# Kernel tuning notes

Hardware: AMD Instinct MI355X
Metric: run time of the kernel (lower is better)

Reference implementation:

```python
import jax, jax.numpy as jnp
import numpy as np

STATE_DIM = 16
CHANNELS = 256
LENGTH = 8192
SAMPLE_RATE = 100.0


def setup_inputs() -> dict:
    key = jax.random.key(0)
    ks = jax.random.split(key, 4)
    fan = 1.0 / np.sqrt(CHANNELS)  # lecun-normal-ish scale, flax Dense default
    x = jax.random.normal(ks[0], (LENGTH, CHANNELS), dtype=jnp.float32)
    logA = jnp.log(1.0 + jnp.arange(STATE_DIM, dtype=jnp.float32))  # module's Ainit
    W_dt = jax.random.normal(ks[1], (CHANNELS, CHANNELS), dtype=jnp.float32) * fan
    b_dt = jnp.zeros((CHANNELS,), dtype=jnp.float32)
    W_B = jax.random.normal(ks[2], (CHANNELS, STATE_DIM), dtype=jnp.float32) * fan
    b_B = jnp.zeros((STATE_DIM,), dtype=jnp.float32)
    W_C = jax.random.normal(ks[3], (CHANNELS, STATE_DIM), dtype=jnp.float32) * fan
    b_C = jnp.zeros((STATE_DIM,), dtype=jnp.float32)
    return {"x": x, "logA": logA, "W_dt": W_dt, "b_dt": b_dt,
            "W_B": W_B, "b_B": b_B, "W_C": W_C, "b_C": b_C}


def reference(x, logA, W_dt, b_dt, W_B, b_B, W_C, b_C):
    # x: (L, C)
    A = -jnp.exp(logA)                                   # (S,)
    dt = jax.nn.softplus(1.0 / SAMPLE_RATE + x @ W_dt + b_dt)  # (L, C)
    B = 1.0 + x @ W_B + b_B                              # (L, S)
    C = x @ W_C + b_C                                    # (L, S)
    # discretize: Adiscr = exp(A * dt), shape (L, C, S)
    Adiscr = jnp.exp(dt[:, :, None] * A[None, None, :])
    # Bdiscr = exp((Adiscr - 1) * (B / A))  (faithful to source, incl. outer exp)
    Bdiscr = jnp.exp((Adiscr - 1.0) * (B / A)[:, None, :])  # (L, C, S)
    u = Bdiscr * x[:, :, None]                           # (L, C, S)

    def ssm_scan(p1, p2):
        (A1, c1), (A2, c2) = p1, p2
        return (A2 * A1, c2 + A2 * c1)

    _, h = jax.lax.associative_scan(ssm_scan, (Adiscr, u))  # h: (L, C, S)
    y = jnp.einsum('ls,lcs->lc', C, h)                    # (L, C)
    return y
```

## Files before the change

kernel.cpp:

```cpp
#include <hip/hip_runtime.h>
#include <hip/hip_bf16.h>
#include <math.h>

#define LL 8192
#define CC 256
#define SS 16
#define NJ (CC*SS)
#define GG 1024
#define TT 8
#define SEGS 16
#define PER (GG/SEGS)

#define LOG2E 1.4426950408889634f
#define LN2   0.6931471805599453f

typedef __attribute__((ext_vector_type(8))) short short8;
typedef __attribute__((ext_vector_type(4))) float floatx4;

__device__ __forceinline__ float fexp2(float v){ return __builtin_amdgcn_exp2f(v); }
__device__ __forceinline__ float flog2v(float v){ return __builtin_amdgcn_logf(v); }

__device__ __forceinline__ float softplus(float z){
    float t = fexp2(-fabsf(z) * LOG2E);
    return fmaxf(z, 0.f) + LN2 * flog2v(1.f + t);
}

__device__ __forceinline__ void load16(float* d, const float* __restrict__ p){
    *(float4*)&d[0]  = *(const float4*)&p[0];
    *(float4*)&d[4]  = *(const float4*)&p[4];
    *(float4*)&d[8]  = *(const float4*)&p[8];
    *(float4*)&d[12] = *(const float4*)&p[12];
}

__device__ __forceinline__ unsigned short f2b(float f){
    __hip_bfloat16 h = __float2bfloat16(f);
    return *(unsigned short*)&h;
}
__device__ __forceinline__ float b2f(unsigned short u){
    __hip_bfloat16 h = *(__hip_bfloat16*)&u;
    return __bfloat162float(h);
}

__global__ __launch_bounds__(256) void k_cast(
    const float* __restrict__ Wdt, const float* __restrict__ WB,
    const float* __restrict__ WC,
    unsigned short* __restrict__ wbh, unsigned short* __restrict__ wbl)
{
    const int idx = blockIdx.x*256 + threadIdx.x;
    const int k = idx & 255;
    const int n = idx >> 8;
    float v;
    if (n < 256)      v = Wdt[(size_t)k*CC + n];
    else if (n < 272) v = WB[(size_t)k*SS + (n-256)];
    else              v = WC[(size_t)k*SS + (n-272)];
    unsigned short hi = f2b(v);
    wbh[(size_t)n*256 + k] = hi;
    wbl[(size_t)n*256 + k] = f2b(v - b2f(hi));
}

#define MBM 64
#define MBN 32
#define MBK 64
#define ASTR 72

__global__ __launch_bounds__(256,4) void k_mm(
    const float* __restrict__ x,
    const unsigned short* __restrict__ wbh, const unsigned short* __restrict__ wbl,
    const float* __restrict__ bdt, const float* __restrict__ bB,
    const float* __restrict__ bC, const float* __restrict__ logA,
    float* __restrict__ dt, float* __restrict__ boa, float* __restrict__ cm)
{
    __shared__ unsigned short Ah[MBM*ASTR];
    __shared__ unsigned short Al[MBM*ASTR];
    __shared__ unsigned short Bh[MBN*ASTR];
    __shared__ unsigned short Bl[MBN*ASTR];

    const int tid  = threadIdx.x;
    const int n0   = blockIdx.x * MBN;
    const int row0 = blockIdx.y * MBM;

    const int lane = tid & 63;
    const int wv   = tid >> 6;
    const int wm   = wv >> 1;
    const int wn   = wv & 1;
    const int m16  = lane & 15;
    const int q    = lane >> 4;

    floatx4 acc[2];
    acc[0] = (floatx4){0.f,0.f,0.f,0.f};
    acc[1] = (floatx4){0.f,0.f,0.f,0.f};

    for (int k0 = 0; k0 < CC; k0 += MBK) {
        __syncthreads();
        #pragma unroll
        for (int h2 = 0; h2 < 2; h2++){
            int chunk = tid + h2*256;
            int r    = chunk >> 3;
            int koff = (chunk & 7) * 8;
            float4 f0 = *(const float4*)&x[(size_t)(row0+r)*CC + k0 + koff];
            float4 f1 = *(const float4*)&x[(size_t)(row0+r)*CC + k0 + koff + 4];
            const float* f = &f0.x;
            float fv[8] = {f0.x,f0.y,f0.z,f0.w,f1.x,f1.y,f1.z,f1.w};
            (void)f;
            unsigned short hs[8], ls[8];
            #pragma unroll
            for (int i=0;i<8;i++){
                hs[i] = f2b(fv[i]);
                ls[i] = f2b(fv[i] - b2f(hs[i]));
            }
            uint4 ph, pl;
            ph.x = (unsigned)hs[0] | ((unsigned)hs[1] << 16);
            ph.y = (unsigned)hs[2] | ((unsigned)hs[3] << 16);
            ph.z = (unsigned)hs[4] | ((unsigned)hs[5] << 16);
            ph.w = (unsigned)hs[6] | ((unsigned)hs[7] << 16);
            pl.x = (unsigned)ls[0] | ((unsigned)ls[1] << 16);
            pl.y = (unsigned)ls[2] | ((unsigned)ls[3] << 16);
            pl.z = (unsigned)ls[4] | ((unsigned)ls[5] << 16);
            pl.w = (unsigned)ls[6] | ((unsigned)ls[7] << 16);
            *(uint4*)&Ah[r*ASTR + koff] = ph;
            *(uint4*)&Al[r*ASTR + koff] = pl;
        }
        {
            int n    = tid >> 3;
            int koff = (tid & 7) * 8;
            *(uint4*)&Bh[n*ASTR + koff] = *(const uint4*)&wbh[(size_t)(n0+n)*256 + k0 + koff];
            *(uint4*)&Bl[n*ASTR + koff] = *(const uint4*)&wbl[(size_t)(n0+n)*256 + k0 + koff];
        }
        __syncthreads();

        #pragma unroll
        for (int ks = 0; ks < MBK; ks += 32) {
            short8 bh = *(const short8*)&Bh[(wn*16 + m16)*ASTR + ks + q*8];
            short8 bl = *(const short8*)&Bl[(wn*16 + m16)*ASTR + ks + q*8];
            #pragma unroll
            for (int mt = 0; mt < 2; mt++){
                short8 ah = *(const short8*)&Ah[(wm*32 + mt*16 + m16)*ASTR + ks + q*8];
                short8 al = *(const short8*)&Al[(wm*32 + mt*16 + m16)*ASTR + ks + q*8];
                acc[mt] = __builtin_amdgcn_mfma_f32_16x16x32_bf16(al, bh, acc[mt], 0, 0, 0);
                acc[mt] = __builtin_amdgcn_mfma_f32_16x16x32_bf16(ah, bl, acc[mt], 0, 0, 0);
                acc[mt] = __builtin_amdgcn_mfma_f32_16x16x32_bf16(ah, bh, acc[mt], 0, 0, 0);
            }
        }
    }

    const int col = n0 + wn*16 + m16;
    if (col < 256) {
        float bias = bdt[col];
        #pragma unroll
        for (int mt = 0; mt < 2; mt++){
            #pragma unroll
            for (int r = 0; r < 4; r++){
                int row = row0 + wm*32 + mt*16 + q*4 + r;
                dt[(size_t)row*CC + col] = softplus(0.01f + acc[mt][r] + bias);
            }
        }
    } else if (col < 272) {
        int s = col - 256;
        float A = -fexp2(logA[s] * LOG2E);
        float sc = LOG2E / A;
        float bias = bB[s];
        #pragma unroll
        for (int mt = 0; mt < 2; mt++){
            #pragma unroll
            for (int r = 0; r < 4; r++){
                int row = row0 + wm*32 + mt*16 + q*4 + r;
                boa[(size_t)row*SS + s] = (1.f + acc[mt][r] + bias) * sc;
            }
        }
    } else {
        int s = col - 272;
        float bias = bC[s];
        #pragma unroll
        for (int mt = 0; mt < 2; mt++){
            #pragma unroll
            for (int r = 0; r < 4; r++){
                int row = row0 + wm*32 + mt*16 + q*4 + r;
                cm[(size_t)row*SS + s] = acc[mt][r] + bias;
            }
        }
    }
}

__global__ __launch_bounds__(256) void k_scan1(const float* __restrict__ dt,
    const float* __restrict__ x, const float* __restrict__ boa,
    const float* __restrict__ logA,
    float* __restrict__ Ap, float* __restrict__ Hl)
{
    const int c = threadIdx.x;
    const int g = blockIdx.x;
    const int row0 = g * TT;

    __shared__ float boS[TT*SS];
    if (c < TT*SS) boS[c] = boa[(size_t)row0*SS + c];

    float Al2[SS];
    #pragma unroll
    for (int s=0;s<SS;s++) Al2[s] = -fexp2(logA[s]*LOG2E) * LOG2E;

    const float* __restrict__ dp = dt + (size_t)row0*CC + c;
    const float* __restrict__ xp = x  + (size_t)row0*CC + c;

    float Apr[SS], h[SS];
    #pragma unroll
    for (int s=0;s<SS;s++){ Apr[s]=1.f; h[s]=0.f; }

    __syncthreads();

    #pragma unroll
    for (int t=0;t<TT;t++){
        float d  = dp[t*CC];
        float xv = xp[t*CC];
        float bo[SS]; load16(bo, &boS[t*SS]);
        #pragma unroll
        for (int s=0;s<SS;s++){
            float a = fexp2(d * Al2[s]);
            float u = fexp2(fmaf(a, bo[s], -bo[s])) * xv;
            h[s] = fmaf(a, h[s], u);
            Apr[s] *= a;
        }
    }

    const size_t base = (size_t)g*NJ + c*SS;
    *(float4*)&Ap[base+0]  = make_float4(Apr[0],Apr[1],Apr[2],Apr[3]);
    *(float4*)&Ap[base+4]  = make_float4(Apr[4],Apr[5],Apr[6],Apr[7]);
    *(float4*)&Ap[base+8]  = make_float4(Apr[8],Apr[9],Apr[10],Apr[11]);
    *(float4*)&Ap[base+12] = make_float4(Apr[12],Apr[13],Apr[14],Apr[15]);
    *(float4*)&Hl[base+0]  = make_float4(h[0],h[1],h[2],h[3]);
    *(float4*)&Hl[base+4]  = make_float4(h[4],h[5],h[6],h[7]);
    *(float4*)&Hl[base+8]  = make_float4(h[8],h[9],h[10],h[11]);
    *(float4*)&Hl[base+12] = make_float4(h[12],h[13],h[14],h[15]);
}

__global__ __launch_bounds__(256) void k_carry(const float* __restrict__ Ap,
    const float* __restrict__ Hl, float* __restrict__ Cr)
{
    const int tid = threadIdx.x;
    const int jl  = tid & 15;
    const int seg = tid >> 4;
    const int j   = blockIdx.x * 16 + jl;

    const size_t base = (size_t)(seg*PER)*NJ + j;

    float Aag = 1.f, Uag = 0.f;
    for (int k0 = 0; k0 < PER; k0 += 8) {
        float a[8], u[8];
        #pragma unroll
        for (int i=0;i<8;i++){
            a[i] = Ap[base + (size_t)(k0+i)*NJ];
            u[i] = Hl[base + (size_t)(k0+i)*NJ];
        }
        #pragma unroll
        for (int i=0;i<8;i++){ Uag = fmaf(a[i], Uag, u[i]); Aag *= a[i]; }
    }

    __shared__ float As[SEGS][17], Us[SEGS][17];
    As[seg][jl] = Aag; Us[seg][jl] = Uag;
    __syncthreads();
    float hin = 0.f;
    for (int t = 0; t < seg; ++t)
        hin = fmaf(As[t][jl], hin, Us[t][jl]);

    float h = hin;
    for (int k0 = 0; k0 < PER; k0 += 8) {
        float a[8], u[8];
        #pragma unroll
        for (int i=0;i<8;i++){
            a[i] = Ap[base + (size_t)(k0+i)*NJ];
            u[i] = Hl[base + (size_t)(k0+i)*NJ];
        }
        #pragma unroll
        for (int i=0;i<8;i++){
            Cr[base + (size_t)(k0+i)*NJ] = h;
            h = fmaf(a[i], h, u[i]);
        }
    }
}

__global__ __launch_bounds__(256) void k_scan2(const float* __restrict__ dt,
    const float* __restrict__ x, const float* __restrict__ boa,
    const float* __restrict__ cmat, const float* __restrict__ logA,
    const float* __restrict__ Cr, float* __restrict__ y)
{
    const int c = threadIdx.x;
    const int g = blockIdx.x;
    const int row0 = g * TT;

    __shared__ float boS[TT*SS], cmS[TT*SS];
    if (c < TT*SS)       boS[c]        = boa [(size_t)row0*SS + c];
    else                 cmS[c-TT*SS]  = cmat[(size_t)row0*SS + (c-TT*SS)];

    float Al2[SS];
    #pragma unroll
    for (int s=0;s<SS;s++) Al2[s] = -fexp2(logA[s]*LOG2E) * LOG2E;

    const float* __restrict__ dp = dt + (size_t)row0*CC + c;
    const float* __restrict__ xp = x  + (size_t)row0*CC + c;
    float* __restrict__ yp = y + (size_t)row0*CC + c;

    float h[SS];
    load16(h, &Cr[(size_t)g*NJ + c*SS]);

    __syncthreads();

    #pragma unroll
    for (int t=0;t<TT;t++){
        float d  = dp[t*CC];
        float xv = xp[t*CC];
        float bo[SS]; load16(bo, &boS[t*SS]);
        float cmv[SS]; load16(cmv, &cmS[t*SS]);
        float yv = 0.f;
        #pragma unroll
        for (int s=0;s<SS;s++){
            float a = fexp2(d * Al2[s]);
            float u = fexp2(fmaf(a, bo[s], -bo[s])) * xv;
            h[s] = fmaf(a, h[s], u);
            yv = fmaf(cmv[s], h[s], yv);
        }
        yp[t*CC] = yv;
    }
}

extern "C" void kernel_launch(void* const* d_in, const int* in_sizes, int n_in,
                              void* d_out, int out_size, void* d_ws, size_t ws_size,
                              hipStream_t stream) {
    const float* x    = (const float*)d_in[0];
    const float* logA = (const float*)d_in[1];
    const float* W_dt = (const float*)d_in[2];
    const float* b_dt = (const float*)d_in[3];
    const float* W_B  = (const float*)d_in[4];
    const float* b_B  = (const float*)d_in[5];
    const float* W_C  = (const float*)d_in[6];
    const float* b_C  = (const float*)d_in[7];
    float* y  = (float*)d_out;
    float* ws = (float*)d_ws;

    float* dt  = ws;
    float* boa = dt  + (size_t)LL*CC;
    float* cmv = boa + (size_t)LL*SS;
    float* Ap  = cmv + (size_t)LL*SS;
    float* Hl  = Ap  + (size_t)GG*NJ;
    float* Cr  = Hl  + (size_t)GG*NJ;
    unsigned short* wbh = (unsigned short*)(Cr + (size_t)GG*NJ);
    unsigned short* wbl = wbh + 288*256;

    hipLaunchKernelGGL(k_cast, dim3(288), dim3(256), 0, stream, W_dt, W_B, W_C, wbh, wbl);
    hipLaunchKernelGGL(k_mm,   dim3(9,128), dim3(256), 0, stream,
                       x, wbh, wbl, b_dt, b_B, b_C, logA, dt, boa, cmv);
    hipLaunchKernelGGL(k_scan1, dim3(GG),    dim3(256), 0, stream,
                       dt, x, boa, logA, Ap, Hl);
    hipLaunchKernelGGL(k_carry, dim3(NJ/16), dim3(256), 0, stream, Ap, Hl, Cr);
    hipLaunchKernelGGL(k_scan2, dim3(GG),    dim3(256), 0, stream,
                       dt, x, boa, cmv, logA, Cr, y);
}
```

Before: 138.6 us.

## Merge chunk scan and carry pass into single-pass decoupled look-back scan

Replaces the k_scan1 and k_carry kernels with one kernel, k_scanA. Each block scans 128 rows for 16 channels using data staged in shared memory, publishes its block aggregate, and then looks back at predecessor blocks through flags to get its incoming carry. It writes per-8-row carries directly. This removes the global round trip of the Ap and Hl intermediates and one kernel launch. In exchange it adds spin-wait synchronisation and a flag memset, and it relies on predecessor blocks being scheduled so that forward progress holds.

```diff
diff --git a/kernel.cpp b/kernel.cpp
--- a/kernel.cpp
+++ b/kernel.cpp
@@ -6,10 +6,11 @@
 #define CC 256
 #define SS 16
 #define NJ (CC*SS)
-#define GG 1024
+#define GG2 1024
 #define TT 8
-#define SEGS 16
-#define PER (GG/SEGS)
+#define GCH 64
+#define CROWS 128
+#define NCB 16
 
 #define LOG2E 1.4426950408889634f
 #define LN2   0.6931471805599453f
@@ -99,9 +100,7 @@
             int koff = (chunk & 7) * 8;
             float4 f0 = *(const float4*)&x[(size_t)(row0+r)*CC + k0 + koff];
             float4 f1 = *(const float4*)&x[(size_t)(row0+r)*CC + k0 + koff + 4];
-            const float* f = &f0.x;
             float fv[8] = {f0.x,f0.y,f0.z,f0.w,f1.x,f1.y,f1.z,f1.w};
-            (void)f;
             unsigned short hs[8], ls[8];
             #pragma unroll
             for (int i=0;i<8;i++){
@@ -181,98 +180,116 @@
     }
 }
 
-__global__ __launch_bounds__(256) void k_scan1(const float* __restrict__ dt,
-    const float* __restrict__ x, const float* __restrict__ boa,
-    const float* __restrict__ logA,
-    float* __restrict__ Ap, float* __restrict__ Hl)
-{
-    const int c = threadIdx.x;
-    const int g = blockIdx.x;
-    const int row0 = g * TT;
-
-    __shared__ float boS[TT*SS];
-    if (c < TT*SS) boS[c] = boa[(size_t)row0*SS + c];
-
-    float Al2[SS];
-    #pragma unroll
-    for (int s=0;s<SS;s++) Al2[s] = -fexp2(logA[s]*LOG2E) * LOG2E;
-
-    const float* __restrict__ dp = dt + (size_t)row0*CC + c;
-    const float* __restrict__ xp = x  + (size_t)row0*CC + c;
-
-    float Apr[SS], h[SS];
-    #pragma unroll
-    for (int s=0;s<SS;s++){ Apr[s]=1.f; h[s]=0.f; }
-
-    __syncthreads();
-
-    #pragma unroll
-    for (int t=0;t<TT;t++){
-        float d  = dp[t*CC];
-        float xv = xp[t*CC];
-        float bo[SS]; load16(bo, &boS[t*SS]);
-        #pragma unroll
-        for (int s=0;s<SS;s++){
-            float a = fexp2(d * Al2[s]);
-            float u = fexp2(fmaf(a, bo[s], -bo[s])) * xv;
-            h[s] = fmaf(a, h[s], u);
-            Apr[s] *= a;
-        }
-    }
-
-    const size_t base = (size_t)g*NJ + c*SS;
-    *(float4*)&Ap[base+0]  = make_float4(Apr[0],Apr[1],Apr[2],Apr[3]);
-    *(float4*)&Ap[base+4]  = make_float4(Apr[4],Apr[5],Apr[6],Apr[7]);
-    *(float4*)&Ap[base+8]  = make_float4(Apr[8],Apr[9],Apr[10],Apr[11]);
-    *(float4*)&Ap[base+12] = make_float4(Apr[12],Apr[13],Apr[14],Apr[15]);
-    *(float4*)&Hl[base+0]  = make_float4(h[0],h[1],h[2],h[3]);
-    *(float4*)&Hl[base+4]  = make_float4(h[4],h[5],h[6],h[7]);
-    *(float4*)&Hl[base+8]  = make_float4(h[8],h[9],h[10],h[11]);
-    *(float4*)&Hl[base+12] = make_float4(h[12],h[13],h[14],h[15]);
-}
-
-__global__ __launch_bounds__(256) void k_carry(const float* __restrict__ Ap,
-    const float* __restrict__ Hl, float* __restrict__ Cr)
+__global__ __launch_bounds__(256) void k_scanA(
+    const float* __restrict__ dt, const float* __restrict__ x,
+    const float* __restrict__ boa, const float* __restrict__ logA,
+    float2* __restrict__ agg, float* __restrict__ pref,
+    int* __restrict__ flags, float* __restrict__ Cr)
 {
     const int tid = threadIdx.x;
-    const int jl  = tid & 15;
-    const int seg = tid >> 4;
-    const int j   = blockIdx.x * 16 + jl;
-
-    const size_t base = (size_t)(seg*PER)*NJ + j;
-
-    float Aag = 1.f, Uag = 0.f;
-    for (int k0 = 0; k0 < PER; k0 += 8) {
-        float a[8], u[8];
-        #pragma unroll
-        for (int i=0;i<8;i++){
-            a[i] = Ap[base + (size_t)(k0+i)*NJ];
-            u[i] = Hl[base + (size_t)(k0+i)*NJ];
-        }
-        #pragma unroll
-        for (int i=0;i<8;i++){ Uag = fmaf(a[i], Uag, u[i]); Aag *= a[i]; }
-    }
-
-    __shared__ float As[SEGS][17], Us[SEGS][17];
-    As[seg][jl] = Aag; Us[seg][jl] = Uag;
+    const int cb  = blockIdx.x;
+    const int g   = blockIdx.y;
+    const int row0 = g * CROWS;
+
+    __shared__ float dtS[CROWS*16], xS[CROWS*16], boS[CROWS*16];
+    __shared__ int sf[4];
+
+    for (int i = tid; i < CROWS*16; i += 256) {
+        int l = i >> 4, ch = i & 15;
+        dtS[i] = dt [(size_t)(row0+l)*CC + cb*16 + ch];
+        xS[i]  = x  [(size_t)(row0+l)*CC + cb*16 + ch];
+        boS[i] = boa[(size_t)(row0+l)*SS + ch];
+    }
+
+    const int cl = tid >> 4;
+    const int s  = tid & 15;
+    const float als = -fexp2(logA[s]*LOG2E) * LOG2E;
+
     __syncthreads();
-    float hin = 0.f;
-    for (int t = 0; t < seg; ++t)
-        hin = fmaf(As[t][jl], hin, Us[t][jl]);
-
-    float h = hin;
-    for (int k0 = 0; k0 < PER; k0 += 8) {
-        float a[8], u[8];
-        #pragma unroll
-        for (int i=0;i<8;i++){
-            a[i] = Ap[base + (size_t)(k0+i)*NJ];
-            u[i] = Hl[base + (size_t)(k0+i)*NJ];
-        }
-        #pragma unroll
-        for (int i=0;i<8;i++){
-            Cr[base + (size_t)(k0+i)*NJ] = h;
-            h = fmaf(a[i], h, u[i]);
-        }
+
+    float subA[16], subU[16];
+    #pragma unroll
+    for (int i=0;i<16;i++){
+        float A = 1.f, U = 0.f;
+        #pragma unroll
+        for (int r=0;r<8;r++){
+            int l = i*8 + r;
+            float d  = dtS[l*16 + cl];
+            float xv = xS [l*16 + cl];
+            float bo = boS[l*16 + s];
+            float a = fexp2(d * als);
+            float u = fexp2(fmaf(a, bo, -bo)) * xv;
+            U = fmaf(a, U, u);
+            A *= a;
+        }
+        subA[i] = A; subU[i] = U;
+    }
+    float Ablk = 1.f, Ublk = 0.f;
+    #pragma unroll
+    for (int i=0;i<16;i++){ Ublk = fmaf(subA[i], Ublk, subU[i]); Ablk *= subA[i]; }
+
+    const int fb = cb * GCH;
+    const size_t myidx = (size_t)(fb + g)*256 + tid;
+
+    if (g > 0) {
+        agg[myidx] = make_float2(Ablk, Ublk);
+        __threadfence();
+        __syncthreads();
+        if (tid == 0)
+            __hip_atomic_store(&flags[fb + g], 1, __ATOMIC_RELEASE, __HIP_MEMORY_SCOPE_AGENT);
+    }
+
+    float c0 = 0.f;
+    if (g > 0) {
+        float accA = 1.f, accU = 0.f;
+        int p = g - 1;
+        bool done = false;
+        while (!done) {
+            if (tid < 4)
+                sf[tid] = (p - tid >= 0)
+                    ? __hip_atomic_load(&flags[fb + p - tid], __ATOMIC_ACQUIRE, __HIP_MEMORY_SCOPE_AGENT)
+                    : 0;
+            __syncthreads();
+            int f0 = sf[0], f1 = sf[1], f2 = sf[2], f3 = sf[3];
+            __syncthreads();
+            if (f0 == 0) { __builtin_amdgcn_s_sleep(2); continue; }
+            float2 av[4]; float pv[4];
+            #pragma unroll
+            for (int i=0;i<4;i++){
+                int pp = p - i; if (pp < 0) pp = 0;
+                size_t idx = (size_t)(fb + pp)*256 + tid;
+                av[i] = agg[idx];
+                pv[i] = pref[idx];
+            }
+            int fl[4] = {f0, f1, f2, f3};
+            int consumed = 0;
+            #pragma unroll
+            for (int i=0;i<4;i++){
+                if (done) continue;
+                int fi = fl[i];
+                if (fi == 0) continue;
+                if (fi >= 2) { c0 = fmaf(accA, pv[i], accU); done = true; }
+                else { accU = fmaf(accA, av[i].y, accU); accA *= av[i].x; consumed++; }
+                if (i < 3 && fl[i+1] == 0 && !done) {  }
+            }
+            p -= consumed;
+        }
+    }
+
+    const int j = cb*256 + tid;
+    float h = c0;
+    #pragma unroll
+    for (int i=0;i<16;i++){
+        Cr[(size_t)(g*16 + i)*NJ + j] = h;
+        h = fmaf(subA[i], h, subU[i]);
+    }
+
+    if (g < GCH-1) {
+        pref[myidx] = h;
+        __threadfence();
+        __syncthreads();
+        if (tid == 0)
+            __hip_atomic_store(&flags[fb + g], 2, __ATOMIC_RELEASE, __HIP_MEMORY_SCOPE_AGENT);
     }
 }
 
@@ -334,21 +351,22 @@
     float* y  = (float*)d_out;
     float* ws = (float*)d_ws;
 
-    float* dt  = ws;
-    float* boa = dt  + (size_t)LL*CC;
-    float* cmv = boa + (size_t)LL*SS;
-    float* Ap  = cmv + (size_t)LL*SS;
-    float* Hl  = Ap  + (size_t)GG*NJ;
-    float* Cr  = Hl  + (size_t)GG*NJ;
-    unsigned short* wbh = (unsigned short*)(Cr + (size_t)GG*NJ);
+    float* dt   = ws;
+    float* boa  = dt   + (size_t)LL*CC;
+    float* cmv  = boa  + (size_t)LL*SS;
+    float* Cr   = cmv  + (size_t)LL*SS;
+    float* prefv= Cr   + (size_t)GG2*NJ;
+    float2* aggv= (float2*)(prefv + (size_t)NCB*GCH*256);
+    unsigned short* wbh = (unsigned short*)(aggv + (size_t)NCB*GCH*256);
     unsigned short* wbl = wbh + 288*256;
-
+    int* flags = (int*)(wbl + 288*256);
+
+    hipMemsetAsync(flags, 0, NCB*GCH*sizeof(int), stream);
     hipLaunchKernelGGL(k_cast, dim3(288), dim3(256), 0, stream, W_dt, W_B, W_C, wbh, wbl);
     hipLaunchKernelGGL(k_mm,   dim3(9,128), dim3(256), 0, stream,
                        x, wbh, wbl, b_dt, b_B, b_C, logA, dt, boa, cmv);
-    hipLaunchKernelGGL(k_scan1, dim3(GG),    dim3(256), 0, stream,
-                       dt, x, boa, logA, Ap, Hl);
-    hipLaunchKernelGGL(k_carry, dim3(NJ/16), dim3(256), 0, stream, Ap, Hl, Cr);
-    hipLaunchKernelGGL(k_scan2, dim3(GG),    dim3(256), 0, stream,
+    hipLaunchKernelGGL(k_scanA, dim3(NCB, GCH), dim3(256), 0, stream,
+                       dt, x, boa, logA, aggv, prefv, flags, Cr);
+    hipLaunchKernelGGL(k_scan2, dim3(GG2), dim3(256), 0, stream,
                        dt, x, boa, cmv, logA, Cr, y);
 }
```

Measured after the change: 354.4 us. +155.7%, slower.

## Precast x to bf16 hi/lo once, double scan chunk length, register-cache carry loads

Applied to the files above, without the earlier changes.

Moves the split of x into bf16 high/low parts out of the matmul tile loop into the cast kernel, so the 9 column-blocks of k_mm read pre-split bf16 instead of reconverting fp32 x each time. Doubles the scan chunk length (TT 8→16, GG 1024→512), halving the Ap/Hl/Cr intermediate traffic. k_carry now loads each segment's a/u values into registers once and reuses them for both passes instead of reading global memory twice. The tradeoffs are an extra write and read of the 2×bf16 x copy, longer serial chains per scan thread, and higher register pressure in k_carry (PER=32 floats per array).

```diff
diff --git a/kernel.cpp b/kernel.cpp
--- a/kernel.cpp
+++ b/kernel.cpp
@@ -6,8 +6,8 @@
 #define CC 256
 #define SS 16
 #define NJ (CC*SS)
-#define GG 1024
-#define TT 8
+#define GG 512
+#define TT 16
 #define SEGS 16
 #define PER (GG/SEGS)
 
@@ -42,20 +42,43 @@
 }
 
 __global__ __launch_bounds__(256) void k_cast(
+    const float* __restrict__ x,
     const float* __restrict__ Wdt, const float* __restrict__ WB,
     const float* __restrict__ WC,
+    unsigned short* __restrict__ xh, unsigned short* __restrict__ xl,
     unsigned short* __restrict__ wbh, unsigned short* __restrict__ wbl)
 {
-    const int idx = blockIdx.x*256 + threadIdx.x;
-    const int k = idx & 255;
-    const int n = idx >> 8;
-    float v;
-    if (n < 256)      v = Wdt[(size_t)k*CC + n];
-    else if (n < 272) v = WB[(size_t)k*SS + (n-256)];
-    else              v = WC[(size_t)k*SS + (n-272)];
-    unsigned short hi = f2b(v);
-    wbh[(size_t)n*256 + k] = hi;
-    wbl[(size_t)n*256 + k] = f2b(v - b2f(hi));
+    const int b = blockIdx.x;
+    if (b < 2048) {
+        const int idx = b*256 + threadIdx.x;
+        const size_t off = (size_t)idx * 4;
+        float4 v = *(const float4*)&x[off];
+        float fv[4] = {v.x, v.y, v.z, v.w};
+        unsigned short hs[4], ls[4];
+        #pragma unroll
+        for (int i=0;i<4;i++){
+            hs[i] = f2b(fv[i]);
+            ls[i] = f2b(fv[i] - b2f(hs[i]));
+        }
+        uint2 ph, pl;
+        ph.x = (unsigned)hs[0] | ((unsigned)hs[1] << 16);
+        ph.y = (unsigned)hs[2] | ((unsigned)hs[3] << 16);
+        pl.x = (unsigned)ls[0] | ((unsigned)ls[1] << 16);
+        pl.y = (unsigned)ls[2] | ((unsigned)ls[3] << 16);
+        *(uint2*)&xh[off] = ph;
+        *(uint2*)&xl[off] = pl;
+    } else {
+        const int idx = (b-2048)*256 + threadIdx.x;
+        const int k = idx & 255;
+        const int n = idx >> 8;
+        float v;
+        if (n < 256)      v = Wdt[(size_t)k*CC + n];
+        else if (n < 272) v = WB[(size_t)k*SS + (n-256)];
+        else              v = WC[(size_t)k*SS + (n-272)];
+        unsigned short hi = f2b(v);
+        wbh[(size_t)n*256 + k] = hi;
+        wbl[(size_t)n*256 + k] = f2b(v - b2f(hi));
+    }
 }
 
 #define MBM 64
@@ -64,7 +87,7 @@
 #define ASTR 72
 
 __global__ __launch_bounds__(256,4) void k_mm(
-    const float* __restrict__ x,
+    const unsigned short* __restrict__ xh, const unsigned short* __restrict__ xl,
     const unsigned short* __restrict__ wbh, const unsigned short* __restrict__ wbl,
     const float* __restrict__ bdt, const float* __restrict__ bB,
     const float* __restrict__ bC, const float* __restrict__ logA,
@@ -94,37 +117,19 @@
         __syncthreads();
         #pragma unroll
         for (int h2 = 0; h2 < 2; h2++){
-            int chunk = tid + h2*256;
-            int r    = chunk >> 3;
-            int koff = (chunk & 7) * 8;
-            float4 f0 = *(const float4*)&x[(size_t)(row0+r)*CC + k0 + koff];
-            float4 f1 = *(const float4*)&x[(size_t)(row0+r)*CC + k0 + koff + 4];
-            const float* f = &f0.x;
-            float fv[8] = {f0.x,f0.y,f0.z,f0.w,f1.x,f1.y,f1.z,f1.w};
-            (void)f;
-            unsigned short hs[8], ls[8];
-            #pragma unroll
-            for (int i=0;i<8;i++){
-                hs[i] = f2b(fv[i]);
-                ls[i] = f2b(fv[i] - b2f(hs[i]));
-            }
-            uint4 ph, pl;
-            ph.x = (unsigned)hs[0] | ((unsigned)hs[1] << 16);
-            ph.y = (unsigned)hs[2] | ((unsigned)hs[3] << 16);
-            ph.z = (unsigned)hs[4] | ((unsigned)hs[5] << 16);
-            ph.w = (unsigned)hs[6] | ((unsigned)hs[7] << 16);
-            pl.x = (unsigned)ls[0] | ((unsigned)ls[1] << 16);
-            pl.y = (unsigned)ls[2] | ((unsigned)ls[3] << 16);
-            pl.z = (unsigned)ls[4] | ((unsigned)ls[5] << 16);
-            pl.w = (unsigned)ls[6] | ((unsigned)ls[7] << 16);
-            *(uint4*)&Ah[r*ASTR + koff] = ph;
-            *(uint4*)&Al[r*ASTR + koff] = pl;
+            int slot = tid + h2*256;
+            int r    = slot >> 3;
+            int koff = (slot & 7) * 8;
+            size_t gix = (size_t)(row0+r)*CC + k0 + koff;
+            *(uint4*)&Ah[r*ASTR + koff] = *(const uint4*)&xh[gix];
+            *(uint4*)&Al[r*ASTR + koff] = *(const uint4*)&xl[gix];
         }
         {
             int n    = tid >> 3;
             int koff = (tid & 7) * 8;
-            *(uint4*)&Bh[n*ASTR + koff] = *(const uint4*)&wbh[(size_t)(n0+n)*256 + k0 + koff];
-            *(uint4*)&Bl[n*ASTR + koff] = *(const uint4*)&wbl[(size_t)(n0+n)*256 + k0 + koff];
+            size_t gix = (size_t)(n0+n)*256 + k0 + koff;
+            *(uint4*)&Bh[n*ASTR + koff] = *(const uint4*)&wbh[gix];
+            *(uint4*)&Bl[n*ASTR + koff] = *(const uint4*)&wbl[gix];
         }
         __syncthreads();
 
@@ -191,7 +196,7 @@
     const int row0 = g * TT;
 
     __shared__ float boS[TT*SS];
-    if (c < TT*SS) boS[c] = boa[(size_t)row0*SS + c];
+    boS[c] = boa[(size_t)row0*SS + c];
 
     float Al2[SS];
     #pragma unroll
@@ -241,17 +246,15 @@
 
     const size_t base = (size_t)(seg*PER)*NJ + j;
 
+    float a[PER], u[PER];
+    #pragma unroll
+    for (int k=0;k<PER;k++){
+        a[k] = Ap[base + (size_t)k*NJ];
+        u[k] = Hl[base + (size_t)k*NJ];
+    }
     float Aag = 1.f, Uag = 0.f;
-    for (int k0 = 0; k0 < PER; k0 += 8) {
-        float a[8], u[8];
-        #pragma unroll
-        for (int i=0;i<8;i++){
-            a[i] = Ap[base + (size_t)(k0+i)*NJ];
-            u[i] = Hl[base + (size_t)(k0+i)*NJ];
-        }
-        #pragma unroll
-        for (int i=0;i<8;i++){ Uag = fmaf(a[i], Uag, u[i]); Aag *= a[i]; }
-    }
+    #pragma unroll
+    for (int k=0;k<PER;k++){ Uag = fmaf(a[k], Uag, u[k]); Aag *= a[k]; }
 
     __shared__ float As[SEGS][17], Us[SEGS][17];
     As[seg][jl] = Aag; Us[seg][jl] = Uag;
@@ -261,18 +264,10 @@
         hin = fmaf(As[t][jl], hin, Us[t][jl]);
 
     float h = hin;
-    for (int k0 = 0; k0 < PER; k0 += 8) {
-        float a[8], u[8];
-        #pragma unroll
-        for (int i=0;i<8;i++){
-            a[i] = Ap[base + (size_t)(k0+i)*NJ];
-            u[i] = Hl[base + (size_t)(k0+i)*NJ];
-        }
-        #pragma unroll
-        for (int i=0;i<8;i++){
-            Cr[base + (size_t)(k0+i)*NJ] = h;
-            h = fmaf(a[i], h, u[i]);
-        }
+    #pragma unroll
+    for (int k=0;k<PER;k++){
+        Cr[base + (size_t)k*NJ] = h;
+        h = fmaf(a[k], h, u[k]);
     }
 }
 
@@ -286,8 +281,8 @@
     const int row0 = g * TT;
 
     __shared__ float boS[TT*SS], cmS[TT*SS];
-    if (c < TT*SS)       boS[c]        = boa [(size_t)row0*SS + c];
-    else                 cmS[c-TT*SS]  = cmat[(size_t)row0*SS + (c-TT*SS)];
+    boS[c] = boa [(size_t)row0*SS + c];
+    cmS[c] = cmat[(size_t)row0*SS + c];
 
     float Al2[SS];
     #pragma unroll
@@ -334,21 +329,24 @@
     float* y  = (float*)d_out;
     float* ws = (float*)d_ws;
 
-    float* dt  = ws;
-    float* boa = dt  + (size_t)LL*CC;
-    float* cmv = boa + (size_t)LL*SS;
-    float* Ap  = cmv + (size_t)LL*SS;
-    float* Hl  = Ap  + (size_t)GG*NJ;
-    float* Cr  = Hl  + (size_t)GG*NJ;
-    unsigned short* wbh = (unsigned short*)(Cr + (size_t)GG*NJ);
+    float* dt   = ws;
+    float* boa  = dt   + (size_t)LL*CC;
+    float* cmv  = boa  + (size_t)LL*SS;
+    float* Ap   = cmv  + (size_t)LL*SS;
+    float* Hl   = Ap   + (size_t)GG*NJ;
+    float* Cr   = Hl   + (size_t)GG*NJ;
+    unsigned short* xh  = (unsigned short*)(Cr + (size_t)GG*NJ);
+    unsigned short* xl  = xh + (size_t)LL*CC;
+    unsigned short* wbh = xl + (size_t)LL*CC;
     unsigned short* wbl = wbh + 288*256;
 
-    hipLaunchKernelGGL(k_cast, dim3(288), dim3(256), 0, stream, W_dt, W_B, W_C, wbh, wbl);
+    hipLaunchKernelGGL(k_cast, dim3(2336), dim3(256), 0, stream,
+                       x, W_dt, W_B, W_C, xh, xl, wbh, wbl);
     hipLaunchKernelGGL(k_mm,   dim3(9,128), dim3(256), 0, stream,
-                       x, wbh, wbl, b_dt, b_B, b_C, logA, dt, boa, cmv);
-    hipLaunchKernelGGL(k_scan1, dim3(GG),    dim3(256), 0, stream,
+                       xh, xl, wbh, wbl, b_dt, b_B, b_C, logA, dt, boa, cmv);
+    hipLaunchKernelGGL(k_scan1, dim3(GG), dim3(256), 0, stream,
                        dt, x, boa, logA, Ap, Hl);
     hipLaunchKernelGGL(k_carry, dim3(NJ/16), dim3(256), 0, stream, Ap, Hl, Cr);
-    hipLaunchKernelGGL(k_scan2, dim3(GG),    dim3(256), 0, stream,
+    hipLaunchKernelGGL(k_scan2, dim3(GG), dim3(256), 0, stream,
                        dt, x, boa, cmv, logA, Cr, y);
 }
```

Result: faster. 129.4 us (-6.6%).
